# Performance work log

Hardware: AMD Instinct MI355X
Metric: run time of the kernel (lower is better)

The kernel has to match this reference:

```python
import jax, jax.numpy as jnp
import numpy as np

N, E = 50000, 800000      # nodes, edges
IN, EF = 128, 64          # node / edge input feature dims
H, F = 4, 16              # heads, out_feats per head
NEG_SLOPE = 0.2


def setup_inputs() -> dict:
    key = jax.random.key(0)
    ks = jax.random.split(key, 11)
    s = 0.1  # xavier-ish scale
    return {
        "feat": jax.random.normal(ks[0], (N, IN), jnp.float32),
        "edge_feat": jax.random.normal(ks[1], (E, EF), jnp.float32),
        "W_fc": jax.random.normal(ks[2], (IN, H * F), jnp.float32) * s,
        "W_edge": jax.random.normal(ks[3], (EF, H * F), jnp.float32) * s,
        "attn_l": jax.random.normal(ks[4], (1, H, F), jnp.float32) * s,
        "attn_r": jax.random.normal(ks[5], (1, H, F), jnp.float32) * s,
        "attn_e": jax.random.normal(ks[6], (1, H, F), jnp.float32) * s,
        "bias": jnp.zeros((H * F,), jnp.float32),
        "W_res": jax.random.normal(ks[7], (IN, H * F), jnp.float32) * s,
        "src": jax.random.randint(ks[8], (E,), 0, N, jnp.int32),
        "dst": jax.random.randint(ks[9], (E,), 0, N, jnp.int32),
    }


def reference(feat, edge_feat, W_fc, W_edge, attn_l, attn_r, attn_e, bias, W_res, src, dst):
    n = feat.shape[0]
    # linear projections -> [N,H,F] / [E,H,F]
    feat_src = (feat @ W_fc).reshape(n, H, F)
    feat_e = (edge_feat @ W_edge).reshape(-1, H, F)
    # per-head attention logits
    el = (feat_src * attn_l).sum(-1)   # [N,H]
    er = (feat_src * attn_r).sum(-1)   # [N,H]
    ee = (feat_e * attn_e).sum(-1)     # [E,H]
    e = jax.nn.leaky_relu(el[src] + er[dst] + ee, NEG_SLOPE)  # [E,H]
    # edge softmax over incoming edges of each dst node (segment softmax)
    emax = jax.ops.segment_max(e, dst, num_segments=n)        # [N,H]
    ex = jnp.exp(e - emax[dst])
    denom = jax.ops.segment_sum(ex, dst, num_segments=n)      # [N,H]
    a = ex / denom[dst]                                       # [E,H]
    # message = (u.ft + e.ft_edge) * a, scatter-sum to dst
    msg = (feat_src[src] + feat_e) * a[..., None]              # [E,H,F]
    rst = jax.ops.segment_sum(msg, dst, num_segments=n)        # [N,H,F]
    # residual + bias
    rst = rst + (feat @ W_res).reshape(n, H, F)
    rst = rst + bias.reshape(1, H, F)
    return rst
```

## Files before the change

### kernel.cpp

```cpp
#include <hip/hip_runtime.h>
#include <hip/hip_bf16.h>
#include <math.h>

#define N_NODES 50000
#define N_EDGES 800000
#define IN_F    128
#define EF_F    64
#define NH      4
#define NF      16
#define HF      64
#define NEG_SLOPE 0.2f

__global__ __launch_bounds__(256) void node_kernel(
    const float* __restrict__ feat,
    const float* __restrict__ W_fc,
    const float* __restrict__ W_res,
    const float* __restrict__ attn_l,
    const float* __restrict__ attn_r,
    const float* __restrict__ bias,
    const int*   __restrict__ dst,
    float* __restrict__ feat_src,
    float* __restrict__ el,
    float* __restrict__ er,
    float* __restrict__ out,
    int*   __restrict__ count)
{
    __shared__ __align__(16) float slot[4][IN_F];

    int gtid = blockIdx.x * 256 + threadIdx.x;
    int gthreads = gridDim.x * 256;
    for (int e = gtid; e < N_EDGES; e += gthreads)
        atomicAdd(&count[dst[e]], 1);

    int lane = threadIdx.x & 63;
    int w    = threadIdx.x >> 6;
    int gw   = blockIdx.x * 4 + w;
    int nwav = gridDim.x * 4;
    int kind = gw & 1;
    int gw2  = gw >> 1;
    int nwav2 = nwav >> 1;

    const float* Wm = kind ? W_res : W_fc;
    float Wc[IN_F];
#pragma unroll
    for (int k = 0; k < IN_F; ++k) Wc[k] = Wm[k * HF + lane];

    float al = attn_l[lane];
    float ar = attn_r[lane];
    float bv = bias[lane];

    for (int n = gw2; n < N_NODES; n += nwav2) {
        slot[w][lane]      = feat[n * IN_F + lane];
        slot[w][lane + 64] = feat[n * IN_F + 64 + lane];
        asm volatile("s_waitcnt lgkmcnt(0)" ::: "memory");

        const float4* s4 = reinterpret_cast<const float4*>(slot[w]);
        float f0 = 0.f, f1 = 0.f, f2 = 0.f, f3 = 0.f;
#pragma unroll
        for (int k4 = 0; k4 < IN_F / 4; ++k4) {
            float4 c = s4[k4];
            f0 += c.x * Wc[k4 * 4 + 0];
            f1 += c.y * Wc[k4 * 4 + 1];
            f2 += c.z * Wc[k4 * 4 + 2];
            f3 += c.w * Wc[k4 * 4 + 3];
        }
        float fs = (f0 + f1) + (f2 + f3);

        if (kind == 0) {
            feat_src[n * HF + lane] = fs;
            float pl = fs * al, pr = fs * ar;
#pragma unroll
            for (int d = 1; d < 16; d <<= 1) {
                pl += __shfl_xor(pl, d, 64);
                pr += __shfl_xor(pr, d, 64);
            }
            if ((lane & 15) == 0) {
                el[n * NH + (lane >> 4)] = pl;
                er[n * NH + (lane >> 4)] = pr;
            }
        } else {
            out[n * HF + lane] = fs + bv;
        }
    }
}

__global__ __launch_bounds__(256) void scan_kernel(
    const int* __restrict__ count,
    int* __restrict__ row_ptr,
    int* __restrict__ cursor)
{
    __shared__ int wsum[4];
    __shared__ int chunk_base;
    int tid = threadIdx.x;
    int lane = tid & 63;
    int w = tid >> 6;
    if (tid == 0) chunk_base = 0;
    __syncthreads();

    for (int base = 0; base < N_NODES; base += 256) {
        int i = base + tid;
        int v = (i < N_NODES) ? count[i] : 0;
        int x = v;
#pragma unroll
        for (int d = 1; d < 64; d <<= 1) {
            int y = __shfl_up(x, d, 64);
            if (lane >= d) x += y;
        }
        if (lane == 63) wsum[w] = x;
        __syncthreads();
        int woff = 0;
        for (int k = 0; k < w; ++k) woff += wsum[k];
        int excl = chunk_base + woff + x - v;
        if (i < N_NODES) { row_ptr[i] = excl; cursor[i] = excl; }
        int total = wsum[0] + wsum[1] + wsum[2] + wsum[3];
        __syncthreads();
        if (tid == 0) chunk_base += total;
        __syncthreads();
    }
    if (threadIdx.x == 0) row_ptr[N_NODES] = N_EDGES;
}

__global__ __launch_bounds__(256) void fill_kernel(
    const int* __restrict__ dst,
    int* __restrict__ cursor,
    int* __restrict__ eids)
{
    int e = blockIdx.x * 256 + threadIdx.x;
    if (e < N_EDGES) {
        int p = atomicAdd(&cursor[dst[e]], 1);
        eids[p] = e;
    }
}

__global__ __launch_bounds__(256) void agg_kernel(
    const float* __restrict__ edge_feat,
    const float* __restrict__ W_edge,
    const float* __restrict__ attn_e,
    const float* __restrict__ feat_src,
    const float* __restrict__ el,
    const float* __restrict__ er,
    const int*   __restrict__ src,
    const int*   __restrict__ row_ptr,
    const int*   __restrict__ eids,
    float* __restrict__ out)
{
    __shared__ __align__(16) float slot[4][2][EF_F];

    int lane = threadIdx.x & 63;
    int w    = threadIdx.x >> 6;
    int h    = lane >> 4;
    int gw   = blockIdx.x * 4 + w;
    int nwav = gridDim.x * 4;

    float Wc[EF_F];
#pragma unroll
    for (int k = 0; k < EF_F; ++k) Wc[k] = W_edge[k * HF + lane];
    float ae = attn_e[lane];

    for (int n = gw; n < N_NODES; n += nwav) {
        int beg = row_ptr[n];
        int end = row_ptr[n + 1];
        float acc = 0.f, m = -1e30f, s = 0.f;
        float er_h = er[n * NH + h];

        int   sv = 0;
        float efv = 0.f, elv = 0.f;
        if (beg < end) {
            int e0 = eids[beg];
            sv  = src[e0];
            efv = edge_feat[e0 * EF_F + lane];
            elv = el[sv * NH + h];
        }

        for (int i = beg; i < end; ++i) {
            int   cur_s  = sv;
            float cur_ef = efv;
            float cur_el = elv;
            int p = i & 1;
            slot[w][p][lane] = cur_ef;

            if (i + 1 < end) {
                int e2 = eids[i + 1];
                sv  = src[e2];
                efv = edge_feat[e2 * EF_F + lane];
                elv = el[sv * NH + h];
            }
            float fsv = feat_src[cur_s * HF + lane];

            asm volatile("s_waitcnt lgkmcnt(0)" ::: "memory");
            const float4* s4 = reinterpret_cast<const float4*>(slot[w][p]);
            float f0 = 0.f, f1 = 0.f, f2 = 0.f, f3 = 0.f;
#pragma unroll
            for (int k4 = 0; k4 < EF_F / 4; ++k4) {
                float4 c = s4[k4];
                f0 += c.x * Wc[k4 * 4 + 0];
                f1 += c.y * Wc[k4 * 4 + 1];
                f2 += c.z * Wc[k4 * 4 + 2];
                f3 += c.w * Wc[k4 * 4 + 3];
            }
            float fe = (f0 + f1) + (f2 + f3);

            float prod = fe * ae;
#pragma unroll
            for (int d = 1; d < 16; d <<= 1) prod += __shfl_xor(prod, d, 64);

            float logit = cur_el + er_h + prod;
            logit = (logit > 0.f) ? logit : NEG_SLOPE * logit;

            float mn = fmaxf(m, logit);
            float sc = __expf(m - mn);
            float pv = __expf(logit - mn);
            s   = s * sc + pv;
            acc = acc * sc + pv * (fsv + fe);
            m   = mn;
        }

        if (beg < end)
            out[n * HF + lane] += acc / s;
    }
}

extern "C" void kernel_launch(void* const* d_in, const int* in_sizes, int n_in,
                              void* d_out, int out_size, void* d_ws, size_t ws_size,
                              hipStream_t stream)
{
    (void)in_sizes; (void)n_in; (void)out_size; (void)ws_size;

    const float* feat      = (const float*)d_in[0];
    const float* edge_feat = (const float*)d_in[1];
    const float* W_fc      = (const float*)d_in[2];
    const float* W_edge    = (const float*)d_in[3];
    const float* attn_l    = (const float*)d_in[4];
    const float* attn_r    = (const float*)d_in[5];
    const float* attn_e    = (const float*)d_in[6];
    const float* bias      = (const float*)d_in[7];
    const float* W_res     = (const float*)d_in[8];
    const int*   src       = (const int*)d_in[9];
    const int*   dst       = (const int*)d_in[10];
    float*       out       = (float*)d_out;

    float* feat_src = (float*)d_ws;
    float* el       = feat_src + (size_t)N_NODES * HF;
    float* er       = el + (size_t)N_NODES * NH;
    int*   count    = (int*)(er + (size_t)N_NODES * NH);
    int*   row_ptr  = count + N_NODES;
    int*   cursor   = row_ptr + N_NODES + 1;
    int*   eids     = cursor + N_NODES;

    hipMemsetAsync(count, 0, N_NODES * sizeof(int), stream);

    node_kernel<<<512, 256, 0, stream>>>(feat, W_fc, W_res, attn_l, attn_r,
                                         bias, dst, feat_src, el, er, out, count);
    scan_kernel<<<1, 256, 0, stream>>>(count, row_ptr, cursor);
    fill_kernel<<<(N_EDGES + 255) / 256, 256, 0, stream>>>(dst, cursor, eids);
    agg_kernel<<<2048, 256, 0, stream>>>(edge_feat, W_edge, attn_e, feat_src,
                                         el, er, src, row_ptr, eids, out);
}
```

Before: 875.7 us.

## Fold edge projection algebraically, precompute edge logits, parallelize CSR scan

Folds W_edge·attn_e into a 64x4 matrix so each edge's logit is computed once in a new per-edge kernel. That kernel also does the in-degree counting and stores exp(logit) per edge. Aggregation now accumulates raw edge features weighted per head and applies W_edge once per node, instead of running a 64x64 matvec per edge. The single-block serial scan becomes a three-kernel block-parallel scan. The online max-subtraction is dropped, which assumes logits stay small enough that exp cannot overflow.

After: 921.0 us. +5.2%, slower.

```diff
diff --git a/kernel.cpp b/kernel.cpp
--- a/kernel.cpp
+++ b/kernel.cpp
@@ -10,6 +10,7 @@
 #define NF      16
 #define HF      64
 #define NEG_SLOPE 0.2f
+#define SCAN_BLOCKS 196
 
 __global__ __launch_bounds__(256) void node_kernel(
     const float* __restrict__ feat,
@@ -17,20 +18,26 @@
     const float* __restrict__ W_res,
     const float* __restrict__ attn_l,
     const float* __restrict__ attn_r,
+    const float* __restrict__ attn_e,
     const float* __restrict__ bias,
-    const int*   __restrict__ dst,
+    const float* __restrict__ W_edge,
     float* __restrict__ feat_src,
     float* __restrict__ el,
     float* __restrict__ er,
     float* __restrict__ out,
-    int*   __restrict__ count)
+    float* __restrict__ Cmat)
 {
     __shared__ __align__(16) float slot[4][IN_F];
 
-    int gtid = blockIdx.x * 256 + threadIdx.x;
-    int gthreads = gridDim.x * 256;
-    for (int e = gtid; e < N_EDGES; e += gthreads)
-        atomicAdd(&count[dst[e]], 1);
+    if (blockIdx.x == 0) {
+        int t = threadIdx.x;
+        int k = t >> 2, h = t & 3;
+        float c = 0.f;
+#pragma unroll
+        for (int f = 0; f < NF; ++f)
+            c += W_edge[k * HF + h * NF + f] * attn_e[h * NF + f];
+        Cmat[t] = c;
+    }
 
     int lane = threadIdx.x & 63;
     int w    = threadIdx.x >> 6;
@@ -84,40 +91,103 @@
     }
 }
 
-__global__ __launch_bounds__(256) void scan_kernel(
-    const int* __restrict__ count,
-    int* __restrict__ row_ptr,
-    int* __restrict__ cursor)
-{
-    __shared__ int wsum[4];
-    __shared__ int chunk_base;
-    int tid = threadIdx.x;
-    int lane = tid & 63;
-    int w = tid >> 6;
-    if (tid == 0) chunk_base = 0;
+__global__ __launch_bounds__(256) void edge_kernel(
+    const float* __restrict__ edge_feat,
+    const float* __restrict__ Cmat,
+    const float* __restrict__ el,
+    const float* __restrict__ er,
+    const int*   __restrict__ src,
+    const int*   __restrict__ dst,
+    float* __restrict__ plog,
+    int*   __restrict__ count)
+{
+    __shared__ __align__(16) float4 Cs[EF_F];
+    int t = threadIdx.x;
+    if (t < EF_F) Cs[t] = ((const float4*)Cmat)[t];
     __syncthreads();
 
-    for (int base = 0; base < N_NODES; base += 256) {
-        int i = base + tid;
-        int v = (i < N_NODES) ? count[i] : 0;
-        int x = v;
-#pragma unroll
-        for (int d = 1; d < 64; d <<= 1) {
-            int y = __shfl_up(x, d, 64);
-            if (lane >= d) x += y;
-        }
-        if (lane == 63) wsum[w] = x;
-        __syncthreads();
-        int woff = 0;
-        for (int k = 0; k < w; ++k) woff += wsum[k];
-        int excl = chunk_base + woff + x - v;
-        if (i < N_NODES) { row_ptr[i] = excl; cursor[i] = excl; }
-        int total = wsum[0] + wsum[1] + wsum[2] + wsum[3];
-        __syncthreads();
-        if (tid == 0) chunk_base += total;
-        __syncthreads();
-    }
-    if (threadIdx.x == 0) row_ptr[N_NODES] = N_EDGES;
+    int e = blockIdx.x * 256 + t;
+    if (e >= N_EDGES) return;
+    int sv = src[e], dv = dst[e];
+    atomicAdd(&count[dv], 1);
+
+    const float4* ef4 = (const float4*)(edge_feat + (size_t)e * EF_F);
+    float4 ee = {0.f, 0.f, 0.f, 0.f};
+#pragma unroll
+    for (int k4 = 0; k4 < EF_F / 4; ++k4) {
+        float4 v = ef4[k4];
+        float4 c;
+        c = Cs[4*k4+0]; ee.x += v.x*c.x; ee.y += v.x*c.y; ee.z += v.x*c.z; ee.w += v.x*c.w;
+        c = Cs[4*k4+1]; ee.x += v.y*c.x; ee.y += v.y*c.y; ee.z += v.y*c.z; ee.w += v.y*c.w;
+        c = Cs[4*k4+2]; ee.x += v.z*c.x; ee.y += v.z*c.y; ee.z += v.z*c.z; ee.w += v.z*c.w;
+        c = Cs[4*k4+3]; ee.x += v.w*c.x; ee.y += v.w*c.y; ee.z += v.w*c.z; ee.w += v.w*c.w;
+    }
+
+    float4 l4 = *(const float4*)(el + (size_t)sv * NH);
+    float4 r4 = *(const float4*)(er + (size_t)dv * NH);
+    float4 p;
+    float g;
+    g = l4.x + r4.x + ee.x; g = (g > 0.f) ? g : NEG_SLOPE * g; p.x = __expf(g);
+    g = l4.y + r4.y + ee.y; g = (g > 0.f) ? g : NEG_SLOPE * g; p.y = __expf(g);
+    g = l4.z + r4.z + ee.z; g = (g > 0.f) ? g : NEG_SLOPE * g; p.z = __expf(g);
+    g = l4.w + r4.w + ee.w; g = (g > 0.f) ? g : NEG_SLOPE * g; p.w = __expf(g);
+    *(float4*)(plog + (size_t)e * NH) = p;
+}
+
+__global__ __launch_bounds__(256) void sum_kernel(
+    const int* __restrict__ count, int* __restrict__ bsum)
+{
+    __shared__ int ws4[4];
+    int i = blockIdx.x * 256 + threadIdx.x;
+    int v = (i < N_NODES) ? count[i] : 0;
+#pragma unroll
+    for (int d = 1; d < 64; d <<= 1) v += __shfl_xor(v, d, 64);
+    if ((threadIdx.x & 63) == 0) ws4[threadIdx.x >> 6] = v;
+    __syncthreads();
+    if (threadIdx.x == 0) bsum[blockIdx.x] = ws4[0] + ws4[1] + ws4[2] + ws4[3];
+}
+
+__global__ __launch_bounds__(256) void scan196_kernel(
+    const int* __restrict__ bsum, int* __restrict__ boff)
+{
+    __shared__ int ws4[4];
+    int t = threadIdx.x;
+    int lane = t & 63, w = t >> 6;
+    int v = (t < SCAN_BLOCKS) ? bsum[t] : 0;
+    int x = v;
+#pragma unroll
+    for (int d = 1; d < 64; d <<= 1) {
+        int y = __shfl_up(x, d, 64);
+        if (lane >= d) x += y;
+    }
+    if (lane == 63) ws4[w] = x;
+    __syncthreads();
+    int off = 0;
+    for (int k = 0; k < w; ++k) off += ws4[k];
+    if (t < SCAN_BLOCKS) boff[t] = off + x - v;
+}
+
+__global__ __launch_bounds__(256) void scatter_kernel(
+    const int* __restrict__ count, const int* __restrict__ boff,
+    int* __restrict__ row_ptr, int* __restrict__ cursor)
+{
+    __shared__ int ws4[4];
+    int i = blockIdx.x * 256 + threadIdx.x;
+    int v = (i < N_NODES) ? count[i] : 0;
+    int lane = threadIdx.x & 63, w = threadIdx.x >> 6;
+    int x = v;
+#pragma unroll
+    for (int d = 1; d < 64; d <<= 1) {
+        int y = __shfl_up(x, d, 64);
+        if (lane >= d) x += y;
+    }
+    if (lane == 63) ws4[w] = x;
+    __syncthreads();
+    int off = boff[blockIdx.x];
+    for (int k = 0; k < w; ++k) off += ws4[k];
+    int excl = off + x - v;
+    if (i < N_NODES) { row_ptr[i] = excl; cursor[i] = excl; }
+    if (i == N_NODES - 1) row_ptr[N_NODES] = excl + v;
 }
 
 __global__ __launch_bounds__(256) void fill_kernel(
@@ -135,16 +205,14 @@
 __global__ __launch_bounds__(256) void agg_kernel(
     const float* __restrict__ edge_feat,
     const float* __restrict__ W_edge,
-    const float* __restrict__ attn_e,
     const float* __restrict__ feat_src,
-    const float* __restrict__ el,
-    const float* __restrict__ er,
+    const float* __restrict__ plog,
     const int*   __restrict__ src,
     const int*   __restrict__ row_ptr,
     const int*   __restrict__ eids,
     float* __restrict__ out)
 {
-    __shared__ __align__(16) float slot[4][2][EF_F];
+    __shared__ __align__(16) float eps[4][NH][68];
 
     int lane = threadIdx.x & 63;
     int w    = threadIdx.x >> 6;
@@ -152,71 +220,89 @@
     int gw   = blockIdx.x * 4 + w;
     int nwav = gridDim.x * 4;
 
-    float Wc[EF_F];
-#pragma unroll
-    for (int k = 0; k < EF_F; ++k) Wc[k] = W_edge[k * HF + lane];
-    float ae = attn_e[lane];
-
     for (int n = gw; n < N_NODES; n += nwav) {
         int beg = row_ptr[n];
         int end = row_ptr[n + 1];
-        float acc = 0.f, m = -1e30f, s = 0.f;
-        float er_h = er[n * NH + h];
-
-        int   sv = 0;
-        float efv = 0.f, elv = 0.f;
-        if (beg < end) {
-            int e0 = eids[beg];
-            sv  = src[e0];
-            efv = edge_feat[e0 * EF_F + lane];
-            elv = el[sv * NH + h];
-        }
-
-        for (int i = beg; i < end; ++i) {
-            int   cur_s  = sv;
-            float cur_ef = efv;
-            float cur_el = elv;
-            int p = i & 1;
-            slot[w][p][lane] = cur_ef;
-
-            if (i + 1 < end) {
-                int e2 = eids[i + 1];
-                sv  = src[e2];
-                efv = edge_feat[e2 * EF_F + lane];
-                elv = el[sv * NH + h];
-            }
-            float fsv = feat_src[cur_s * HF + lane];
-
-            asm volatile("s_waitcnt lgkmcnt(0)" ::: "memory");
-            const float4* s4 = reinterpret_cast<const float4*>(slot[w][p]);
-            float f0 = 0.f, f1 = 0.f, f2 = 0.f, f3 = 0.f;
-#pragma unroll
-            for (int k4 = 0; k4 < EF_F / 4; ++k4) {
-                float4 c = s4[k4];
-                f0 += c.x * Wc[k4 * 4 + 0];
-                f1 += c.y * Wc[k4 * 4 + 1];
-                f2 += c.z * Wc[k4 * 4 + 2];
-                f3 += c.w * Wc[k4 * 4 + 3];
-            }
-            float fe = (f0 + f1) + (f2 + f3);
-
-            float prod = fe * ae;
-#pragma unroll
-            for (int d = 1; d < 16; d <<= 1) prod += __shfl_xor(prod, d, 64);
-
-            float logit = cur_el + er_h + prod;
-            logit = (logit > 0.f) ? logit : NEG_SLOPE * logit;
-
-            float mn = fmaxf(m, logit);
-            float sc = __expf(m - mn);
-            float pv = __expf(logit - mn);
-            s   = s * sc + pv;
-            acc = acc * sc + pv * (fsv + fe);
-            m   = mn;
-        }
-
-        if (beg < end)
-            out[n * HF + lane] += acc / s;
+        if (beg == end) continue;
+
+        float  accf = 0.f;
+        float4 acce = {0.f, 0.f, 0.f, 0.f};
+        float4 s4   = {0.f, 0.f, 0.f, 0.f};
+
+        float efA = 0.f, fsA = 0.f; float4 pA = {0.f,0.f,0.f,0.f};
+        float efB = 0.f, fsB = 0.f; float4 pB = {0.f,0.f,0.f,0.f};
+        {
+            int e = eids[beg]; int sv = src[e];
+            efA = edge_feat[(size_t)e * HF + lane];
+            fsA = feat_src[(size_t)sv * HF + lane];
+            pA  = *(const float4*)(plog + (size_t)e * NH);
+        }
+        if (beg + 1 < end) {
+            int e = eids[beg + 1]; int sv = src[e];
+            efB = edge_feat[(size_t)e * HF + lane];
+            fsB = feat_src[(size_t)sv * HF + lane];
+            pB  = *(const float4*)(plog + (size_t)e * NH);
+        }
+
+        int i = beg;
+        for (; i + 1 < end; i += 2) {
+            {
+                float ph = (h & 2) ? ((h & 1) ? pA.w : pA.z)
+                                   : ((h & 1) ? pA.y : pA.x);
+                s4.x += pA.x; s4.y += pA.y; s4.z += pA.z; s4.w += pA.w;
+                accf += ph * fsA;
+                acce.x += pA.x * efA; acce.y += pA.y * efA;
+                acce.z += pA.z * efA; acce.w += pA.w * efA;
+            }
+            if (i + 2 < end) {
+                int e = eids[i + 2]; int sv = src[e];
+                efA = edge_feat[(size_t)e * HF + lane];
+                fsA = feat_src[(size_t)sv * HF + lane];
+                pA  = *(const float4*)(plog + (size_t)e * NH);
+            }
+            {
+                float ph = (h & 2) ? ((h & 1) ? pB.w : pB.z)
+                                   : ((h & 1) ? pB.y : pB.x);
+                s4.x += pB.x; s4.y += pB.y; s4.z += pB.z; s4.w += pB.w;
+                accf += ph * fsB;
+                acce.x += pB.x * efB; acce.y += pB.y * efB;
+                acce.z += pB.z * efB; acce.w += pB.w * efB;
+            }
+            if (i + 3 < end) {
+                int e = eids[i + 3]; int sv = src[e];
+                efB = edge_feat[(size_t)e * HF + lane];
+                fsB = feat_src[(size_t)sv * HF + lane];
+                pB  = *(const float4*)(plog + (size_t)e * NH);
+            }
+        }
+        if (i < end) {
+            float ph = (h & 2) ? ((h & 1) ? pA.w : pA.z)
+                               : ((h & 1) ? pA.y : pA.x);
+            s4.x += pA.x; s4.y += pA.y; s4.z += pA.z; s4.w += pA.w;
+            accf += ph * fsA;
+            acce.x += pA.x * efA; acce.y += pA.y * efA;
+            acce.z += pA.z * efA; acce.w += pA.w * efA;
+        }
+
+        eps[w][0][lane] = acce.x;
+        eps[w][1][lane] = acce.y;
+        eps[w][2][lane] = acce.z;
+        eps[w][3][lane] = acce.w;
+        asm volatile("s_waitcnt lgkmcnt(0)" ::: "memory");
+
+        const float4* row = (const float4*)(&eps[w][h][0]);
+        float fe = 0.f;
+#pragma unroll
+        for (int k4 = 0; k4 < EF_F / 4; ++k4) {
+            float4 a4 = row[k4];
+            fe += a4.x * W_edge[(k4 * 4 + 0) * HF + lane];
+            fe += a4.y * W_edge[(k4 * 4 + 1) * HF + lane];
+            fe += a4.z * W_edge[(k4 * 4 + 2) * HF + lane];
+            fe += a4.w * W_edge[(k4 * 4 + 3) * HF + lane];
+        }
+        float sh = (h & 2) ? ((h & 1) ? s4.w : s4.z)
+                           : ((h & 1) ? s4.y : s4.x);
+        out[(size_t)n * HF + lane] += (accf + fe) / sh;
     }
 }
 
@@ -242,17 +328,26 @@
     float* feat_src = (float*)d_ws;
     float* el       = feat_src + (size_t)N_NODES * HF;
     float* er       = el + (size_t)N_NODES * NH;
-    int*   count    = (int*)(er + (size_t)N_NODES * NH);
+    float* plog     = er + (size_t)N_NODES * NH;
+    float* Cmat     = plog + (size_t)N_EDGES * NH;
+    int*   count    = (int*)(Cmat + 256);
     int*   row_ptr  = count + N_NODES;
     int*   cursor   = row_ptr + N_NODES + 1;
     int*   eids     = cursor + N_NODES;
+    int*   bsum     = eids + N_EDGES;
+    int*   boff     = bsum + SCAN_BLOCKS;
 
     hipMemsetAsync(count, 0, N_NODES * sizeof(int), stream);
 
     node_kernel<<<512, 256, 0, stream>>>(feat, W_fc, W_res, attn_l, attn_r,
-                                         bias, dst, feat_src, el, er, out, count);
-    scan_kernel<<<1, 256, 0, stream>>>(count, row_ptr, cursor);
+                                         attn_e, bias, W_edge,
+                                         feat_src, el, er, out, Cmat);
+    edge_kernel<<<(N_EDGES + 255) / 256, 256, 0, stream>>>(edge_feat, Cmat, el, er,
+                                                           src, dst, plog, count);
+    sum_kernel<<<SCAN_BLOCKS, 256, 0, stream>>>(count, bsum);
+    scan196_kernel<<<1, 256, 0, stream>>>(bsum, boff);
+    scatter_kernel<<<SCAN_BLOCKS, 256, 0, stream>>>(count, boff, row_ptr, cursor);
     fill_kernel<<<(N_EDGES + 255) / 256, 256, 0, stream>>>(dst, cursor, eids);
-    agg_kernel<<<2048, 256, 0, stream>>>(edge_feat, W_edge, attn_e, feat_src,
-                                         el, er, src, row_ptr, eids, out);
-}
+    agg_kernel<<<2048, 256, 0, stream>>>(edge_feat, W_edge, feat_src, plog,
+                                         src, row_ptr, eids, out);
+}
```
